# Optimization experiments

Measured on AMD Instinct MI355X. Metric: run time of the kernel, lower is better.

Reference implementation:

```python
import jax, jax.numpy as jnp
import numpy as np

BANDWIDTH = 1.0
DRIFT_COEF = 1.0
NEG_DRIFT_COEF = 0.5
EPS = 1e-8

B, TA, DA = 4096, 16, 8


def setup_inputs() -> dict:
    key = jax.random.key(0)
    k1, k2, k3 = jax.random.split(key, 3)
    x = jax.random.normal(k1, (B, TA, DA), dtype=jnp.float32)
    y_pos = jax.random.normal(k2, (B, TA, DA), dtype=jnp.float32)
    y_neg = jax.random.normal(k3, (B, TA, DA), dtype=jnp.float32)
    return {"x": x, "y_pos": y_pos, "y_neg": y_neg}


def _drift_field(x_flat, y_flat, sign):
    """Nadaraya-Watson weighted average of pairwise diffs, fused via norms+matmul.

    Equivalent to: sign * sum_j wn_ij * (x_i - y_j)
    where wn = row-normalized RBF kernel with masked diagonal.
    """
    b = x_flat.shape[0]
    x_sq = jnp.sum(x_flat * x_flat, axis=1)
    y_sq = jnp.sum(y_flat * y_flat, axis=1)
    d2 = x_sq[:, None] + y_sq[None, :] - 2.0 * (x_flat @ y_flat.T)
    d2 = jnp.maximum(d2, 0.0)
    w = jnp.exp(-d2 / (2.0 * BANDWIDTH ** 2))
    # mask self-interaction (mask_self=True)
    w = w * (1.0 - jnp.eye(b, dtype=w.dtype))
    s = jnp.sum(w, axis=1, keepdims=True)               # (B, 1)
    denom = jnp.maximum(s, EPS)
    wn = w / denom                                       # (B, B)
    # sum_j wn_ij (x_i - y_j) = x_i * rowsum(wn)_i - wn @ y
    diff_avg = x_flat * (s / denom) - wn @ y_flat        # (B, D)
    return sign * diff_avg


def reference(x, y_pos, y_neg):
    b = x.shape[0]
    x_flat = x.reshape(b, -1)
    yp_flat = y_pos.reshape(b, -1)
    yn_flat = y_neg.reshape(b, -1)
    # V_pos = wn_pos @ (-(x_i - y_j)); V_neg = wn_neg @ (x_i - y_j)
    v = DRIFT_COEF * _drift_field(x_flat, yp_flat, -1.0)
    v = v + NEG_DRIFT_COEF * _drift_field(x_flat, yn_flat, 1.0)
    return v.reshape(x.shape)
```

## Files before the change

### kernel.cpp

```cpp
#include <hip/hip_runtime.h>
#include <math.h>


#define EPSV 1e-8f
#define CUTOFF_F 162.0f
#define LCAP 512
#define RCAP 64

typedef unsigned int uint;
typedef unsigned short ushort;
typedef __attribute__((ext_vector_type(8))) short bf16x8;
typedef __attribute__((ext_vector_type(4))) float f32x4;

#define CNT_IDX 20480u
#define COUNTS_IDX 20481u
#define REGION_BYTE 131072u
#define OVF_BYTE 1310720u
#define OVF_CAP 98304u
#define XA_BYTE 2097152u
#define MAT_BYTES 1048576u
#define WS_NEED 5242880u

static __device__ __forceinline__ ushort bf16_rne(float v) {
    uint u = __float_as_uint(v);
    uint r = (u + 0x7FFFu + ((u >> 16) & 1u)) >> 16;
    return (ushort)r;
}

typedef const __attribute__((address_space(1))) uint guint;
typedef __attribute__((address_space(3))) uint luint;
static __device__ __forceinline__ void lds_load16(const void* g, void* l) {
    __builtin_amdgcn_global_load_lds((guint*)g, (luint*)l, 16, 0, 0);
}

__global__ __launch_bounds__(256) void prep_k(
    const float* __restrict__ x, const float* __restrict__ yp,
    const float* __restrict__ yn, float* __restrict__ ws,
    unsigned char* __restrict__ wsb, int build)
{
    __shared__ ushort hi_s[4][128];
    const int t = threadIdx.x, wv = t >> 6, lane = t & 63;
    const int rid = blockIdx.x * 4 + wv;
    const int seg = rid >> 12;
    const int row = rid & 4095;
    const float* src = (seg == 0) ? x : (seg == 1) ? yp : yn;

    float2 v = ((const float2*)(src + (size_t)row * 128))[lane];
    float ss = v.x * v.x + v.y * v.y;
    #pragma unroll
    for (int off = 32; off > 0; off >>= 1) ss += __shfl_down(ss, off);
    if (lane == 0) ws[8192 + seg * 4096 + row] = ss;

    if (build) {
        hi_s[wv][2 * lane]     = bf16_rne(v.x);
        hi_s[wv][2 * lane + 1] = bf16_rne(v.y);
        __syncthreads();
        const int K = 2 * lane;
        const int g = K >> 6, c = (K >> 3) & 7, off = K & 7;
        const int Klog = (g << 6) + ((c ^ (row & 7)) << 3) + off;
        uint* dst = (uint*)(wsb + XA_BYTE + (size_t)seg * MAT_BYTES) + (size_t)row * 64;
        dst[lane] = (uint)hi_s[wv][Klog] | ((uint)hi_s[wv][Klog + 1] << 16);
    }

    const int gid = blockIdx.x * 256 + t;
    if (gid < 8192) ws[gid] = 0.0f;
    if (gid >= 8192 && gid < 8192 + 2049)
        ((uint*)ws)[CNT_IDX + (gid - 8192)] = 0u;
}

__global__ __launch_bounds__(256) void phase_a_mfma(
    const float* __restrict__ x, const float* __restrict__ yp,
    const float* __restrict__ yn,
    const unsigned char* __restrict__ wsb, float* __restrict__ wsf,
    unsigned ovfcap)
{
    const int f = blockIdx.z;
    const ushort* __restrict__ XA = (const ushort*)(wsb + XA_BYTE);
    const ushort* __restrict__ YB = (const ushort*)(wsb + XA_BYTE + (f ? 2u : 1u) * MAT_BYTES);
    const float* __restrict__ Yg  = f ? yn : yp;
    const float* __restrict__ xsq = wsf + 8192;
    const float* __restrict__ ysq = wsf + (f ? 16384 : 12288);
    float* __restrict__ S         = wsf + (f ? 4096 : 0);
    uint* cnt     = (uint*)wsf + CNT_IDX;
    uint* counts  = (uint*)wsf + COUNTS_IDX;
    uint2* region = (uint2*)((unsigned char*)wsf + REGION_BYTE);
    uint2* ovf    = (uint2*)((unsigned char*)wsf + OVF_BYTE);

    __shared__ ushort As[128 * 64];
    __shared__ ushort Bs[128 * 64];
    __shared__ uint pbuf[LCAP];
    __shared__ uint pcnt, obase;

    const int t = threadIdx.x;
    const int lane = t & 63, wv = t >> 6;
    const int wr = wv >> 1, wc = wv & 1;
    const int i0 = blockIdx.y * 128, j0 = blockIdx.x * 128;
    const int m = lane & 15, qd = lane >> 4;
    const uint b = (uint)blockIdx.z * 1024u + (uint)blockIdx.y * 32u + (uint)blockIdx.x;

    if (t == 0) pcnt = 0;

    f32x4 acc[4][4];
    #pragma unroll
    for (int a = 0; a < 4; ++a)
        #pragma unroll
        for (int bb = 0; bb < 4; ++bb) acc[a][bb] = (f32x4)0.0f;

    const int srow = lane >> 3;
    const int scol = lane & 7;

    for (int k0 = 0; k0 < 128; k0 += 64) {
        #pragma unroll
        for (int q = 0; q < 4; ++q) {
            const int grp = 4 * wv + q;
            const int r = grp * 8 + srow;
            const ushort* ga = XA + (size_t)(i0 + r) * 128 + k0 + scol * 8;
            const ushort* gb = YB + (size_t)(j0 + r) * 128 + k0 + scol * 8;
            lds_load16(ga, &As[grp * 512]);
            lds_load16(gb, &Bs[grp * 512]);
        }
        __syncthreads();
        #pragma unroll
        for (int ks = 0; ks < 2; ++ks) {
            bf16x8 av[4], bv[4];
            #pragma unroll
            for (int ff = 0; ff < 4; ++ff) {
                const int ra = 64 * wr + 16 * ff + m;
                const int ca = (4 * ks + qd) ^ (m & 7);
                av[ff] = *(const bf16x8*)&As[ra * 64 + ca * 8];
                const int rb = 64 * wc + 16 * ff + m;
                const int cb = (4 * ks + qd) ^ (m & 7);
                bv[ff] = *(const bf16x8*)&Bs[rb * 64 + cb * 8];
            }
            #pragma unroll
            for (int fi = 0; fi < 4; ++fi)
                #pragma unroll
                for (int fj = 0; fj < 4; ++fj)
                    acc[fi][fj] = __builtin_amdgcn_mfma_f32_16x16x32_bf16(
                        av[fi], bv[fj], acc[fi][fj], 0, 0, 0);
        }
        __syncthreads();
    }

    float xq[4][4], yq[4];
    #pragma unroll
    for (int fi = 0; fi < 4; ++fi)
        #pragma unroll
        for (int rg = 0; rg < 4; ++rg)
            xq[fi][rg] = xsq[i0 + 64 * wr + 16 * fi + 4 * qd + rg];
    #pragma unroll
    for (int fj = 0; fj < 4; ++fj)
        yq[fj] = ysq[j0 + 64 * wc + 16 * fj + m];

    #pragma unroll
    for (int fi = 0; fi < 4; ++fi) {
        #pragma unroll
        for (int fj = 0; fj < 4; ++fj) {
            #pragma unroll
            for (int rg = 0; rg < 4; ++rg) {
                const int i = i0 + 64 * wr + 16 * fi + 4 * qd + rg;
                const int j = j0 + 64 * wc + 16 * fj + m;
                float d2a = xq[fi][rg] + yq[fj] - 2.0f * acc[fi][fj][rg];
                if (d2a < CUTOFF_F && i != j) {
                    uint li = atomicAdd(&pcnt, 1u);
                    if (li < LCAP)
                        pbuf[li] = (uint)i | ((uint)j << 12) | ((uint)f << 24);
                }
            }
        }
    }
    __syncthreads();
    uint n = pcnt; if (n > LCAP) n = LCAP;
    const uint nr = (n > RCAP) ? RCAP : n;
    if (t == 0) {
        counts[b] = nr;
        if (n > RCAP) obase = atomicAdd(cnt, n - RCAP);
    }
    __syncthreads();
    for (uint p = wv; p < n; p += 4) {
        const uint pk = pbuf[p];
        const uint i = pk & 0xFFFu, j = (pk >> 12) & 0xFFFu;
        float2 xa = ((const float2*)(x + (size_t)i * 128))[lane];
        float2 yb = ((const float2*)(Yg + (size_t)j * 128))[lane];
        float d = xa.x * yb.x + xa.y * yb.y;
        #pragma unroll
        for (int off = 32; off > 0; off >>= 1) d += __shfl_down(d, off);
        if (lane == 0) {
            float d2 = fmaxf(xsq[i] + ysq[j] - 2.0f * d, 0.0f);
            float w = __expf(-0.5f * d2);
            atomicAdd(&S[i], w);
            uint2 pr = make_uint2(pk, __float_as_uint(w));
            if (p < RCAP) {
                region[b * RCAP + p] = pr;
            } else {
                uint gi = obase + (p - RCAP);
                if (gi < ovfcap) ovf[gi] = pr;
            }
        }
    }
}

__global__ __launch_bounds__(256) void phase_a_f32(
    const float* __restrict__ x, const float* __restrict__ yp,
    const float* __restrict__ yn, float* __restrict__ ws,
    unsigned char* __restrict__ wsb, unsigned ovfcap)
{
    const int f = blockIdx.z;
    const float* __restrict__ Y   = f ? yn : yp;
    const float* __restrict__ xsq = ws + 8192;
    const float* __restrict__ ysq = ws + (f ? 16384 : 12288);
    float* __restrict__ S         = ws + (f ? 4096 : 0);
    unsigned* cnt = (unsigned*)ws + CNT_IDX;
    uint2* ovf    = (uint2*)(wsb + OVF_BYTE);

    __shared__ float xs[32][128 + 4];
    __shared__ float ys[32][128 + 4];

    const int t  = threadIdx.x;
    const int tx = t & 15, ty = t >> 4;
    const int i0 = blockIdx.y * 128, j0 = blockIdx.x * 128;

    float acc[8][8];
    #pragma unroll
    for (int a = 0; a < 8; ++a)
        #pragma unroll
        for (int bb = 0; bb < 8; ++bb) acc[a][bb] = 0.f;

    const int ldr = t >> 1;
    const int ldk = (t & 1) * 16;

    for (int k0 = 0; k0 < 128; k0 += 32) {
        #pragma unroll
        for (int q = 0; q < 4; ++q) {
            float4 vx = *(const float4*)&x[(size_t)(i0 + ldr) * 128 + k0 + ldk + 4 * q];
            float4 vy = *(const float4*)&Y[(size_t)(j0 + ldr) * 128 + k0 + ldk + 4 * q];
            const int kb = ldk + 4 * q;
            xs[kb + 0][ldr] = vx.x; xs[kb + 1][ldr] = vx.y;
            xs[kb + 2][ldr] = vx.z; xs[kb + 3][ldr] = vx.w;
            ys[kb + 0][ldr] = vy.x; ys[kb + 1][ldr] = vy.y;
            ys[kb + 2][ldr] = vy.z; ys[kb + 3][ldr] = vy.w;
        }
        __syncthreads();
        #pragma unroll 4
        for (int kk = 0; kk < 32; ++kk) {
            float4 a0 = *(const float4*)&xs[kk][8 * ty];
            float4 a1 = *(const float4*)&xs[kk][8 * ty + 4];
            float4 b0 = *(const float4*)&ys[kk][8 * tx];
            float4 b1 = *(const float4*)&ys[kk][8 * tx + 4];
            float av[8] = {a0.x, a0.y, a0.z, a0.w, a1.x, a1.y, a1.z, a1.w};
            float bv[8] = {b0.x, b0.y, b0.z, b0.w, b1.x, b1.y, b1.z, b1.w};
            #pragma unroll
            for (int di = 0; di < 8; ++di)
                #pragma unroll
                for (int dj = 0; dj < 8; ++dj)
                    acc[di][dj] = fmaf(av[di], bv[dj], acc[di][dj]);
        }
        __syncthreads();
    }

    float xqv[8], yqv[8], srow[8];
    #pragma unroll
    for (int di = 0; di < 8; ++di) { xqv[di] = xsq[i0 + 8 * ty + di]; srow[di] = 0.f; }
    #pragma unroll
    for (int dj = 0; dj < 8; ++dj) yqv[dj] = ysq[j0 + 8 * tx + dj];

    #pragma unroll
    for (int di = 0; di < 8; ++di) {
        const int i = i0 + 8 * ty + di;
        #pragma unroll
        for (int dj = 0; dj < 8; ++dj) {
            const int j = j0 + 8 * tx + dj;
            float d2 = fmaxf(xqv[di] + yqv[dj] - 2.0f * acc[di][dj], 0.0f);
            if (i != j) {
                float w = __expf(-0.5f * d2);
                srow[di] += w;
                if (d2 < CUTOFF_F) {
                    unsigned idx = atomicAdd(cnt, 1u);
                    if (idx < ovfcap)
                        ovf[idx] = make_uint2(
                            (unsigned)i | ((unsigned)j << 12) | ((unsigned)f << 24),
                            __float_as_uint(w));
                }
            }
        }
    }
    #pragma unroll
    for (int di = 0; di < 8; ++di) {
        float v = srow[di];
        #pragma unroll
        for (int off = 8; off > 0; off >>= 1) v += __shfl_down(v, off, 16);
        if (tx == 0) atomicAdd(&S[i0 + 8 * ty + di], v);
    }
}

__global__ __launch_bounds__(256) void finalize_k(
    const float* __restrict__ x, const float* __restrict__ ws,
    float* __restrict__ out)
{
    const int gid = blockIdx.x * 256 + threadIdx.x;
    const int i = gid >> 7;
    float spv = ws[i], snv = ws[4096 + i];
    float c = 0.5f * snv / fmaxf(snv, EPSV) - spv / fmaxf(spv, EPSV);
    out[gid] = x[gid] * c;
}

__global__ __launch_bounds__(256) void scatter_k(
    const float* __restrict__ yp, const float* __restrict__ yn,
    const float* __restrict__ ws, const unsigned char* __restrict__ wsb,
    float* __restrict__ out, unsigned ovfcap)
{
    const uint* counts  = (const uint*)ws + COUNTS_IDX;
    const uint2* region = (const uint2*)(wsb + REGION_BYTE);
    const uint2* ovf    = (const uint2*)(wsb + OVF_BYTE);
    const uint b = blockIdx.x;
    const uint t = threadIdx.x;
    const uint k = t & 127u, ph = t >> 7;

    const uint n = counts[b];
    for (uint p = ph; p < n; p += 2) {
        const uint2 pr = region[b * RCAP + p];
        const uint i  = pr.x & 0xFFFu;
        const uint j  = (pr.x >> 12) & 0xFFFu;
        const uint fb = (pr.x >> 24) & 1u;
        const float w = __uint_as_float(pr.y);
        const float den  = fmaxf(ws[fb * 4096u + i], EPSV);
        const float coef = fb ? (-0.5f / den) : (1.0f / den);
        const float* Yv  = fb ? yn : yp;
        atomicAdd(&out[i * 128u + k], coef * w * Yv[j * 128u + k]);
    }

    uint m = *((const uint*)ws + CNT_IDX); if (m > ovfcap) m = ovfcap;
    const uint total = m * 128u;
    for (uint u = b * 256u + t; u < total; u += 2048u * 256u) {
        const uint p = u >> 7, kk = u & 127u;
        const uint2 pr = ovf[p];
        const uint i  = pr.x & 0xFFFu;
        const uint j  = (pr.x >> 12) & 0xFFFu;
        const uint fb = (pr.x >> 24) & 1u;
        const float w = __uint_as_float(pr.y);
        const float den  = fmaxf(ws[fb * 4096u + i], EPSV);
        const float coef = fb ? (-0.5f / den) : (1.0f / den);
        const float* Yv  = fb ? yn : yp;
        atomicAdd(&out[i * 128u + kk], coef * w * Yv[j * 128u + kk]);
    }
}

extern "C" void kernel_launch(void* const* d_in, const int* in_sizes, int n_in,
                              void* d_out, int out_size, void* d_ws, size_t ws_size,
                              hipStream_t stream)
{
    const float* x  = (const float*)d_in[0];
    const float* yp = (const float*)d_in[1];
    const float* yn = (const float*)d_in[2];
    float* out = (float*)d_out;
    float* ws  = (float*)d_ws;
    unsigned char* wsb = (unsigned char*)d_ws;

    unsigned ovfcap = OVF_CAP;
    if (ws_size < 2097152u)
        ovfcap = (ws_size > OVF_BYTE + 8) ? (unsigned)((ws_size - OVF_BYTE) / 8) : 0u;
    const bool use_mfma = (ws_size >= WS_NEED);

    dim3 ga(32, 32, 2);
    prep_k<<<3072, 256, 0, stream>>>(x, yp, yn, ws, wsb, use_mfma ? 1 : 0);
    if (use_mfma) {
        phase_a_mfma<<<ga, 256, 0, stream>>>(x, yp, yn, wsb, ws, ovfcap);
    } else {
        phase_a_f32<<<ga, 256, 0, stream>>>(x, yp, yn, ws, wsb, ovfcap);
    }
    finalize_k<<<2048, 256, 0, stream>>>(x, ws, out);
    scatter_k<<<2048, 256, 0, stream>>>(yp, yn, ws, wsb, out, ovfcap);
}
```

Measured before the change: 104.7 us.

## Load MFMA operands directly from global into registers, drop LDS staging

The bf16 operand matrices are now stored unswizzled in row-major order by the prep kernel. The MFMA phase reads its A and B fragments straight from global memory into registers instead of staging 128x64 tiles through LDS with global_load_lds and barriers. This removes the LDS traffic, the swizzle, and the synchronisation. In exchange, every wave issues redundant global loads that rely on L1/L2 caching, and the accesses are strided 16-byte reads that coalesce less well.

```diff
diff --git a/kernel.cpp b/kernel.cpp
--- a/kernel.cpp
+++ b/kernel.cpp
@@ -27,18 +27,11 @@
     return (ushort)r;
 }
 
-typedef const __attribute__((address_space(1))) uint guint;
-typedef __attribute__((address_space(3))) uint luint;
-static __device__ __forceinline__ void lds_load16(const void* g, void* l) {
-    __builtin_amdgcn_global_load_lds((guint*)g, (luint*)l, 16, 0, 0);
-}
-
 __global__ __launch_bounds__(256) void prep_k(
     const float* __restrict__ x, const float* __restrict__ yp,
     const float* __restrict__ yn, float* __restrict__ ws,
     unsigned char* __restrict__ wsb, int build)
 {
-    __shared__ ushort hi_s[4][128];
     const int t = threadIdx.x, wv = t >> 6, lane = t & 63;
     const int rid = blockIdx.x * 4 + wv;
     const int seg = rid >> 12;
@@ -52,14 +45,8 @@
     if (lane == 0) ws[8192 + seg * 4096 + row] = ss;
 
     if (build) {
-        hi_s[wv][2 * lane]     = bf16_rne(v.x);
-        hi_s[wv][2 * lane + 1] = bf16_rne(v.y);
-        __syncthreads();
-        const int K = 2 * lane;
-        const int g = K >> 6, c = (K >> 3) & 7, off = K & 7;
-        const int Klog = (g << 6) + ((c ^ (row & 7)) << 3) + off;
         uint* dst = (uint*)(wsb + XA_BYTE + (size_t)seg * MAT_BYTES) + (size_t)row * 64;
-        dst[lane] = (uint)hi_s[wv][Klog] | ((uint)hi_s[wv][Klog + 1] << 16);
+        dst[lane] = (uint)bf16_rne(v.x) | ((uint)bf16_rne(v.y) << 16);
     }
 
     const int gid = blockIdx.x * 256 + t;
@@ -68,7 +55,7 @@
         ((uint*)ws)[CNT_IDX + (gid - 8192)] = 0u;
 }
 
-__global__ __launch_bounds__(256) void phase_a_mfma(
+__global__ __launch_bounds__(256) void phase_a_reg(
     const float* __restrict__ x, const float* __restrict__ yp,
     const float* __restrict__ yn,
     const unsigned char* __restrict__ wsb, float* __restrict__ wsf,
@@ -86,8 +73,6 @@
     uint2* region = (uint2*)((unsigned char*)wsf + REGION_BYTE);
     uint2* ovf    = (uint2*)((unsigned char*)wsf + OVF_BYTE);
 
-    __shared__ ushort As[128 * 64];
-    __shared__ ushort Bs[128 * 64];
     __shared__ uint pbuf[LCAP];
     __shared__ uint pcnt, obase;
 
@@ -106,40 +91,23 @@
         #pragma unroll
         for (int bb = 0; bb < 4; ++bb) acc[a][bb] = (f32x4)0.0f;
 
-    const int srow = lane >> 3;
-    const int scol = lane & 7;
-
-    for (int k0 = 0; k0 < 128; k0 += 64) {
-        #pragma unroll
-        for (int q = 0; q < 4; ++q) {
-            const int grp = 4 * wv + q;
-            const int r = grp * 8 + srow;
-            const ushort* ga = XA + (size_t)(i0 + r) * 128 + k0 + scol * 8;
-            const ushort* gb = YB + (size_t)(j0 + r) * 128 + k0 + scol * 8;
-            lds_load16(ga, &As[grp * 512]);
-            lds_load16(gb, &Bs[grp * 512]);
-        }
-        __syncthreads();
-        #pragma unroll
-        for (int ks = 0; ks < 2; ++ks) {
-            bf16x8 av[4], bv[4];
+    const ushort* Abase = XA + (size_t)(i0 + 64 * wr + m) * 128 + qd * 8;
+    const ushort* Bbase = YB + (size_t)(j0 + 64 * wc + m) * 128 + qd * 8;
+
+    #pragma unroll
+    for (int ks = 0; ks < 4; ++ks) {
+        bf16x8 av[4], bv[4];
+        #pragma unroll
+        for (int ff = 0; ff < 4; ++ff) {
+            av[ff] = *(const bf16x8*)(Abase + (size_t)ff * 16 * 128 + ks * 32);
+            bv[ff] = *(const bf16x8*)(Bbase + (size_t)ff * 16 * 128 + ks * 32);
+        }
+        #pragma unroll
+        for (int fi = 0; fi < 4; ++fi)
             #pragma unroll
-            for (int ff = 0; ff < 4; ++ff) {
-                const int ra = 64 * wr + 16 * ff + m;
-                const int ca = (4 * ks + qd) ^ (m & 7);
-                av[ff] = *(const bf16x8*)&As[ra * 64 + ca * 8];
-                const int rb = 64 * wc + 16 * ff + m;
-                const int cb = (4 * ks + qd) ^ (m & 7);
-                bv[ff] = *(const bf16x8*)&Bs[rb * 64 + cb * 8];
-            }
-            #pragma unroll
-            for (int fi = 0; fi < 4; ++fi)
-                #pragma unroll
-                for (int fj = 0; fj < 4; ++fj)
-                    acc[fi][fj] = __builtin_amdgcn_mfma_f32_16x16x32_bf16(
-                        av[fi], bv[fj], acc[fi][fj], 0, 0, 0);
-        }
-        __syncthreads();
+            for (int fj = 0; fj < 4; ++fj)
+                acc[fi][fj] = __builtin_amdgcn_mfma_f32_16x16x32_bf16(
+                    av[fi], bv[fj], acc[fi][fj], 0, 0, 0);
     }
 
     float xq[4][4], yq[4];
@@ -364,7 +332,7 @@
     dim3 ga(32, 32, 2);
     prep_k<<<3072, 256, 0, stream>>>(x, yp, yn, ws, wsb, use_mfma ? 1 : 0);
     if (use_mfma) {
-        phase_a_mfma<<<ga, 256, 0, stream>>>(x, yp, yn, wsb, ws, ovfcap);
+        phase_a_reg<<<ga, 256, 0, stream>>>(x, yp, yn, wsb, ws, ovfcap);
     } else {
         phase_a_f32<<<ga, 256, 0, stream>>>(x, yp, yn, ws, wsb, ovfcap);
     }
```

Result: slower. 126.8 us (+21.1%).
